# Performance work log

Hardware: AMD Instinct MI355X
Metric: run time of the kernel (lower is better)

## Reference

```python
import jax, jax.numpy as jnp
from jax import lax
import numpy as np

P = 16          # patch_len
EPS = 1e-5      # BatchNorm eps


def _dct_mats(L):
    # torch_dct DCT-II: ortho matrix Co and scale d s.t. dct(norm=None)(x) = (x @ Co.T) * d,
    # dct(norm='ortho')(x) = x @ Co.T, idct(norm=None)(y) = (y / d) @ Co
    n = jnp.arange(L, dtype=jnp.float32)
    base = jnp.cos(jnp.pi * (2.0 * n[None, :] + 1.0) * n[:, None] / (2.0 * L))
    ck = jnp.where(n == 0, 1.0 / jnp.sqrt(jnp.float32(L)), jnp.sqrt(2.0 / L))
    Co = base * ck[:, None]
    d = jnp.where(n == 0, 2.0 * jnp.sqrt(jnp.float32(L)), jnp.sqrt(2.0 * L))
    return Co, d


def _gelu(t):
    return jax.nn.gelu(t, approximate=False)  # torch nn.GELU default (erf)


def _dw(t, w, pad):  # depthwise Conv1d, t [B,D,L], w [D,k], SAME-style padding
    return lax.conv_general_dilated(t, w[:, None, :], (1,), [(pad, pad)],
                                    feature_group_count=t.shape[1],
                                    dimension_numbers=('NCH', 'OIH', 'NCH'))


def _forward(x, conv1_w, conv1_b, conv2_w, conv2_b, conv3_w, conv3_b,
             dn_g, dn_b, dn_m, dn_v, pn_g, pn_b, pn_m, pn_v,
             embed_w, embed_b, lin_res_w, lin_res_b,
             depth_res_w, depth_res_b, depth_conv_w, depth_conv_b,
             threshold, att_dw_w, att_dw_b, att_conv_w, att_conv_b,
             att_g, att_b, att_m, att_v, fc1_w, fc1_b, fc2_w, fc2_b):
    B, L, D = x.shape
    N = L // P                       # patch_num (stride == patch_len)
    Co, dvec = _dct_mats(L)

    conv1 = lambda t: t * conv1_w[:, None] + conv1_b[:, None]   # grouped 1x1 Conv1d
    bnD = lambda t: (t - dn_m[:, None]) * (dn_g[:, None] / jnp.sqrt(dn_v[:, None] + EPS)) + dn_b[:, None]

    xt = jnp.transpose(x, (0, 2, 1))                 # [B,D,L]
    freq_res = conv1(xt)
    z_dct = (xt @ Co.T) * dvec                       # dct(norm=None)

    # adaptive high-frequency mask
    energy = jnp.sum(z_dct * z_dct, axis=-1)         # [B,D]
    med = jnp.median(energy, axis=1, keepdims=True)
    ne = energy / (med + 1e-6)
    thr = lax.stop_gradient(jnp.quantile(ne, jnp.clip(threshold[0], 0.0, 1.0)))
    mask = (ne > thr).astype(x.dtype)[..., None]     # rows of dominant vars -> 1
    z = _gelu(conv1(z_dct * mask))
    z1 = (z / dvec) @ Co + freq_res                  # idct(norm=None) + residual

    # patching (stride == patch_len -> unfold is a reshape)
    z_p = xt.reshape(B * D, N, P) @ embed_w + embed_b            # [BD,N,P*P]
    z_res = (z_p.reshape(B, D, -1) @ lin_res_w + lin_res_b).transpose(0, 2, 1)  # [B,pred,D]
    time_res = z_p @ depth_res_w + depth_res_b                   # [BD,N,P]
    # depth_conv: grouped Conv1d kernel=stride=P over d_model=P*P
    z_depth = jnp.einsum('bnpj,nj->bnp', z_p.reshape(B * D, N, P, P), depth_conv_w) \
              + depth_conv_b[None, :, None] + time_res
    z_depth = (z_depth - pn_m[:, None]) * (pn_g[:, None] / jnp.sqrt(pn_v[:, None] + EPS)) + pn_b[:, None]
    z2 = _gelu(z_depth).reshape(B, D, L)

    z2_f = conv1(bnD(_gelu((z2 @ Co.T) * dvec)))

    z_r = jax.nn.sigmoid(conv1(bnD(_gelu(_dw(z1, conv2_w, 2) + conv2_b[:, None]))))
    zg = _gelu(z2_f * z_r)

    z1b = _gelu(bnD(_dw(z1, conv3_w, 3) + conv3_b[:, None]))
    z1c = bnD(zg) + z1b

    # DctAtt on z1c * z2: ortho DCT, take 5 low-freq comps per var
    xa = (z1c * z2) @ Co.T                            # [B,D,L]
    low = xa[:, :, :5].reshape(B, D, 5)               # concat layout matches torch loop
    zd = jnp.einsum('bdj,j->bd', low, att_dw_w) + att_dw_b[0]   # Conv1d(1,1,5,stride=5)
    zd = _gelu(zd)
    zd = (zd - att_m[0]) * (att_g[0] / jnp.sqrt(att_v[0] + EPS)) + att_b[0]  # BN(1)
    zd = zd * att_conv_w[0] + att_conv_b[0]           # Conv1d(1,1,1)
    att1 = jax.nn.softmax(zd, axis=-1)[..., None]     # [B,D,1]

    zf = z1c * att1 + z2 * (1.0 - att1)
    out = _gelu(zf @ fc1_w + fc1_b) @ fc2_w + fc2_b   # Mlp -> [B,D,pred]
    return z_res + out.transpose(0, 2, 1)             # [B,pred,D]


def setup_inputs() -> dict:
    key = jax.random.key(0)
    ks = iter(jax.random.split(key, 48))
    B, L, D, pred = 32, 512, 321, 96
    N, dm = L // P, P * P
    r = lambda shape, s=1.0: jax.random.normal(next(ks), shape, jnp.float32) * s
    return dict(
        x=r((B, L, D)),
        conv1_w=r((D,), 0.5) + 1.0, conv1_b=r((D,), 0.1),
        conv2_w=r((D, 5), 0.3), conv2_b=r((D,), 0.1),
        conv3_w=r((D, 7), 0.3), conv3_b=r((D,), 0.1),
        dn_g=jnp.ones((D,), jnp.float32), dn_b=jnp.zeros((D,), jnp.float32),
        dn_m=r((D,), 0.1), dn_v=jnp.ones((D,), jnp.float32),
        pn_g=jnp.ones((N,), jnp.float32), pn_b=jnp.zeros((N,), jnp.float32),
        pn_m=r((N,), 0.1), pn_v=jnp.ones((N,), jnp.float32),
        embed_w=r((P, dm), 0.25), embed_b=r((dm,), 0.02),
        lin_res_w=r((N * dm, pred), 0.01), lin_res_b=r((pred,), 0.02),
        depth_res_w=r((dm, P), 0.06), depth_res_b=r((P,), 0.02),
        depth_conv_w=r((N, P), 0.25), depth_conv_b=r((N,), 0.02),
        threshold=jax.random.uniform(next(ks), (1,), jnp.float32) * 0.5,
        att_dw_w=r((5,), 0.4), att_dw_b=r((1,), 0.1),
        att_conv_w=r((1,)), att_conv_b=r((1,), 0.1),
        att_g=jnp.ones((1,), jnp.float32), att_b=jnp.zeros((1,), jnp.float32),
        att_m=jnp.zeros((1,), jnp.float32), att_v=jnp.ones((1,), jnp.float32),
        fc1_w=r((L, pred), 0.04), fc1_b=r((pred,), 0.02),
        fc2_w=r((pred, pred), 0.1), fc2_b=r((pred,), 0.02),
    )


def reference(x, conv1_w, conv1_b, conv2_w, conv2_b, conv3_w, conv3_b,
              dn_g, dn_b, dn_m, dn_v, pn_g, pn_b, pn_m, pn_v,
              embed_w, embed_b, lin_res_w, lin_res_b,
              depth_res_w, depth_res_b, depth_conv_w, depth_conv_b,
              threshold, att_dw_w, att_dw_b, att_conv_w, att_conv_b,
              att_g, att_b, att_m, att_v, fc1_w, fc1_b, fc2_w, fc2_b):
    return _forward(x, conv1_w, conv1_b, conv2_w, conv2_b, conv3_w, conv3_b,
                    dn_g, dn_b, dn_m, dn_v, pn_g, pn_b, pn_m, pn_v,
                    embed_w, embed_b, lin_res_w, lin_res_b,
                    depth_res_w, depth_res_b, depth_conv_w, depth_conv_b,
                    threshold, att_dw_w, att_dw_b, att_conv_w, att_conv_b,
                    att_g, att_b, att_m, att_v, fc1_w, fc1_b, fc2_w, fc2_b)
```

## Files before the change

kernel.cpp:

```cpp
#include <hip/hip_runtime.h>
#include <cmath>


#define BB   32
#define LL   512
#define DD   321
#define PRED 96
#define M_ROWS (BB*DD)

__device__ __forceinline__ float gelu_f(float x){
  return 0.5f*x*(1.0f + erff(x*0.70710678118654752440f));
}
__device__ __forceinline__ float sigmoid_f(float x){
  return 1.0f/(1.0f+expf(-x));
}

constexpr size_t OFF_CO   = 0;
constexpr size_t OFF_COT  = OFF_CO   + 512*512;
constexpr size_t OFF_DVEC = OFF_COT  + 512*512;
constexpr size_t OFF_CATT = OFF_DVEC + 512;
constexpr size_t OFF_FC1T = OFF_CATT + 512;
constexpr size_t OFF_WEFFT= OFF_FC1T + 96*512;
constexpr size_t OFF_CRES = OFF_WEFFT+ 96*512;
constexpr size_t OFF_MP   = OFF_CRES + 128;
constexpr size_t OFF_C2P  = OFF_MP   + 32*256;
constexpr size_t OFF_AF   = OFF_C2P  + 512;
constexpr size_t OFF_CF   = OFF_AF   + 384;
constexpr size_t OFF_DNS  = OFF_CF   + 384;
constexpr size_t OFF_BF   = OFF_DNS  + 384;
constexpr size_t OFF_EN   = OFF_BF   + 384;
constexpr size_t OFF_NE   = OFF_EN   + 10368;
constexpr size_t OFF_THR  = OFF_NE   + 10368;
constexpr size_t OFF_ZDP  = OFF_THR  + 64;
constexpr size_t OFF_ATT1 = OFF_ZDP  + 10368;
constexpr size_t OFF_XT   = OFF_ATT1 + 10368;
constexpr size_t OFF_ZDCT = OFF_XT   + (size_t)M_ROWS*512;
constexpr size_t OFF_Z1   = OFF_ZDCT + (size_t)M_ROWS*512;
constexpr size_t OFF_Z2   = OFF_Z1   + (size_t)M_ROWS*512;
constexpr size_t OFF_Z1C  = OFF_Z2   + (size_t)M_ROWS*512;
constexpr size_t OFF_H    = OFF_Z1C  + (size_t)M_ROWS*512;
constexpr size_t OFF_ZRES = OFF_H    + (size_t)M_ROWS*96;
constexpr size_t WS_FLOATS= OFF_ZRES + (size_t)M_ROWS*96;

__global__ __launch_bounds__(256)
void k0_dct(float* __restrict__ Co, float* __restrict__ CoT, float* __restrict__ dvec,
            float* __restrict__ catt, const float* __restrict__ attw)
{
  const float PI_F = 3.14159265358979323846f;
  int b = blockIdx.x;
  float ckb = (b==0) ? (1.0f/sqrtf(512.0f)) : sqrtf(2.0f/512.0f);
  for (int l=threadIdx.x; l<512; l+=256){
    float a1 = PI_F * (float)(2*l+1);
    float a2 = a1 * (float)b;
    float c  = cosf(a2 * (1.0f/1024.0f)) * ckb;
    Co[b*512+l] = c;
  }
  for (int k=threadIdx.x; k<512; k+=256){
    float ckk = (k==0) ? (1.0f/sqrtf(512.0f)) : sqrtf(2.0f/512.0f);
    float a1 = PI_F * (float)(2*b+1);
    float a2 = a1 * (float)k;
    CoT[b*512+k] = cosf(a2 * (1.0f/1024.0f)) * ckk;
  }
  if (threadIdx.x==0) dvec[b] = (b==0) ? 2.0f*sqrtf(512.0f) : sqrtf(2.0f*512.0f);
  if (b==0){
    for (int l=threadIdx.x; l<512; l+=256){
      float sacc=0.f;
      for (int j=0;j<5;j++){
        float ckj = (j==0)?(1.0f/sqrtf(512.0f)):sqrtf(2.0f/512.0f);
        float a1 = PI_F*(float)(2*l+1);
        float a2 = a1*(float)j;
        sacc += cosf(a2 * (1.0f/1024.0f))*ckj*attw[j];
      }
      catt[l]=sacc;
    }
  }
}

__global__ __launch_bounds__(128)
void k0_weff(const float* __restrict__ embed_w, const float* __restrict__ embed_b,
             const float* __restrict__ lrw, const float* __restrict__ lrb,
             const float* __restrict__ fc1_w,
             float* __restrict__ fc1T, float* __restrict__ WeffT, float* __restrict__ cres)
{
  int l = blockIdx.x; int pr = threadIdx.x;
  if (l < 512){
    if (pr < 96){
      int n = l>>4, p = l&15;
      float a0=0.f,a1=0.f,a2=0.f,a3=0.f;
      for (int j=0;j<256;j+=4){
        a0 = fmaf(embed_w[p*256+j+0], lrw[((size_t)(n*256+j+0))*96+pr], a0);
        a1 = fmaf(embed_w[p*256+j+1], lrw[((size_t)(n*256+j+1))*96+pr], a1);
        a2 = fmaf(embed_w[p*256+j+2], lrw[((size_t)(n*256+j+2))*96+pr], a2);
        a3 = fmaf(embed_w[p*256+j+3], lrw[((size_t)(n*256+j+3))*96+pr], a3);
      }
      WeffT[pr*512 + l] = (a0+a1)+(a2+a3);
      fc1T [pr*512 + l] = fc1_w[l*96+pr];
    }
  } else {
    if (pr < 96){
      float a0=lrb[pr], a1=0.f, a2=0.f, a3=0.f;
      for (int i=0;i<8192;i+=4){
        a0 = fmaf(embed_b[(i+0) & 255], lrw[(size_t)(i+0)*96+pr], a0);
        a1 = fmaf(embed_b[(i+1) & 255], lrw[(size_t)(i+1)*96+pr], a1);
        a2 = fmaf(embed_b[(i+2) & 255], lrw[(size_t)(i+2)*96+pr], a2);
        a3 = fmaf(embed_b[(i+3) & 255], lrw[(size_t)(i+3)*96+pr], a3);
      }
      cres[pr]=(a0+a1)+(a2+a3);
    }
  }
}

__global__ __launch_bounds__(256)
void k0_depth(const float* __restrict__ embed_w, const float* __restrict__ embed_b,
              const float* __restrict__ drw, const float* __restrict__ drb,
              const float* __restrict__ dcw, const float* __restrict__ dcb,
              const float* __restrict__ png, const float* __restrict__ pnb,
              const float* __restrict__ pnm, const float* __restrict__ pnv,
              float* __restrict__ Mp, float* __restrict__ c2p)
{
  int n = blockIdx.x; int tid = threadIdx.x;
  int q = tid>>4, p = tid&15;
  float acc = 0.f;
  for (int j=0;j<16;j++)  acc = fmaf(embed_w[q*256 + p*16 + j], dcw[n*16+j], acc);
  float wtr = 0.f;
  for (int j=0;j<256;j++) wtr = fmaf(embed_w[q*256 + j], drw[j*16+p], wtr);
  float sn = png[n]/sqrtf(pnv[n]+1e-5f);
  Mp[n*256 + q*16 + p] = (acc + wtr) * sn;
  if (q==0){
    float c = dcb[n];
    for (int j=0;j<16;j++)  c = fmaf(embed_b[p*16+j], dcw[n*16+j], c);
    float ctr = drb[p];
    for (int j=0;j<256;j++) ctr = fmaf(embed_b[j], drw[j*16+p], ctr);
    c += ctr;
    c2p[n*16+p] = (c - pnm[n])*sn + pnb[n];
  }
}

__global__ void k0_fold(const float* __restrict__ w1, const float* __restrict__ b1,
                        const float* __restrict__ g,  const float* __restrict__ bbq,
                        const float* __restrict__ mq, const float* __restrict__ vq,
                        float* __restrict__ Af, float* __restrict__ Cf,
                        float* __restrict__ dns, float* __restrict__ Bf)
{
  int d = blockIdx.x*256 + threadIdx.x;
  if (d >= DD) return;
  float s  = g[d]/sqrtf(vq[d]+1e-5f);
  float bf = bbq[d] - mq[d]*s;
  dns[d]=s; Bf[d]=bf; Af[d]=s*w1[d]; Cf[d]=bf*w1[d]+b1[d];
}

__global__ __launch_bounds__(256)
void k1_transpose(const float* __restrict__ x, float* __restrict__ xt)
{
  int b = blockIdx.z; int l0 = blockIdx.y*32; int d0 = blockIdx.x*32;
  __shared__ float t[32][33];
  int tid=threadIdx.x; int j = tid&31, i0 = tid>>5;
  for (int ii=0; ii<32; ii+=8){
    int l = l0 + i0+ii; int d = d0 + j;
    t[i0+ii][j] = (d<DD) ? x[((size_t)b*512 + l)*DD + d] : 0.f;
  }
  __syncthreads();
  for (int ii=0; ii<32; ii+=8){
    int d = d0 + i0+ii; int l = l0 + j;
    if (d<DD) xt[((size_t)b*DD+d)*512 + l] = t[j][i0+ii];
  }
}

template<int OP>
__global__ __launch_bounds__(256)
void gemm_nt(const float* __restrict__ A, const float* __restrict__ B,
             float* __restrict__ C, int M, int Ncols, int ldc,
             const float* __restrict__ p0, const float* __restrict__ p1,
             const float* __restrict__ p2, const float* __restrict__ p3)
{
  __shared__ float As[32][132];
  __shared__ float Bs[32][68];
  const int tid = threadIdx.x;
  const int tx = tid & 15, ty = tid >> 4;
  const int rb = blockIdx.y * 128, cb = blockIdx.x * 64;

  float acc[8][4];
  #pragma unroll
  for (int i=0;i<8;i++)
    #pragma unroll
    for (int j=0;j<4;j++) acc[i][j]=0.f;

  for (int kb=0; kb<512; kb+=32){
    #pragma unroll
    for (int i=0;i<4;i++){
      int idx = tid + i*256;
      int row = idx >> 3, k4 = (idx & 7)*4;
      float4 v = make_float4(0.f,0.f,0.f,0.f);
      int r = rb + row;
      if (r < M) v = *reinterpret_cast<const float4*>(A + (size_t)r*512 + kb + k4);
      As[k4+0][row]=v.x; As[k4+1][row]=v.y; As[k4+2][row]=v.z; As[k4+3][row]=v.w;
    }
    #pragma unroll
    for (int i=0;i<2;i++){
      int idx = tid + i*256;
      int row = idx >> 3, k4 = (idx & 7)*4;
      float4 v = make_float4(0.f,0.f,0.f,0.f);
      int c = cb + row;
      if (c < Ncols) v = *reinterpret_cast<const float4*>(B + (size_t)c*512 + kb + k4);
      Bs[k4+0][row]=v.x; Bs[k4+1][row]=v.y; Bs[k4+2][row]=v.z; Bs[k4+3][row]=v.w;
    }
    __syncthreads();
    #pragma unroll
    for (int kk=0; kk<32; kk++){
      const float4 a0 = *reinterpret_cast<const float4*>(&As[kk][ty*8]);
      const float4 a1 = *reinterpret_cast<const float4*>(&As[kk][ty*8+4]);
      const float4 b0 = *reinterpret_cast<const float4*>(&Bs[kk][tx*4]);
      float av[8]={a0.x,a0.y,a0.z,a0.w,a1.x,a1.y,a1.z,a1.w};
      float bv[4]={b0.x,b0.y,b0.z,b0.w};
      #pragma unroll
      for (int i=0;i<8;i++)
        #pragma unroll
        for (int j=0;j<4;j++) acc[i][j]=fmaf(av[i],bv[j],acc[i][j]);
    }
    __syncthreads();
  }

  #pragma unroll
  for (int i=0;i<8;i++){
    const int r = rb + ty*8 + i;
    const bool rok = (r < M);
    if constexpr (OP==0){
      if (rok){
        #pragma unroll
        for (int j=0;j<4;j++){
          int c = cb + tx*4 + j;
          C[(size_t)r*ldc + c] = acc[i][j]*p0[c];
        }
      }
    } else if constexpr (OP==1){
      if (rok){
        int d = r % DD;
        float w = p0[d], bo = p1[d];
        #pragma unroll
        for (int j=0;j<4;j++){
          int c = cb + tx*4 + j;
          C[(size_t)r*ldc + c] = acc[i][j] + p2[(size_t)r*512 + c]*w + bo;
        }
      }
    } else if constexpr (OP==2){
      if (rok){
        int d = r % DD;
        float w = p0[d], bo = p1[d];
        #pragma unroll
        for (int j=0;j<4;j++){
          int c = cb + tx*4 + j;
          float t = acc[i][j]*p3[c];
          C[(size_t)r*ldc + c] = gelu_f(t)*w + bo;
        }
      }
    } else if constexpr (OP==3){
      if (rok){
        #pragma unroll
        for (int j=0;j<4;j++){
          int c = cb + tx*4 + j;
          if (c < Ncols) C[(size_t)r*ldc + c] = gelu_f(acc[i][j] + p0[c]);
        }
      }
    } else {
      if (rok){
        #pragma unroll
        for (int j=0;j<4;j++){
          int c = cb + tx*4 + j;
          if (c < Ncols) C[(size_t)r*ldc + c] = acc[i][j] + p0[c];
        }
      }
    }
  }
}

__global__ __launch_bounds__(256)
void k_energy(const float* __restrict__ zdct, float* __restrict__ energy)
{
  int r=blockIdx.x, tid=threadIdx.x;
  __shared__ float rbuf[256];
  float acc=0.f;
  for (int k=tid;k<512;k+=256){ float v=zdct[(size_t)r*512+k]; acc=fmaf(v,v,acc); }
  rbuf[tid]=acc; __syncthreads();
  for (int st=128;st>0;st>>=1){ if(tid<st) rbuf[tid]+=rbuf[tid+st]; __syncthreads(); }
  if (tid==0) energy[r]=rbuf[0];
}

__global__ __launch_bounds__(256)
void k3_median(const float* __restrict__ energy, float* __restrict__ ne)
{
  int b = blockIdx.x, tid=threadIdx.x;
  __shared__ float e[DD];
  __shared__ float medv;
  for (int i=tid;i<DD;i+=256) e[i]=energy[b*DD+i];
  __syncthreads();
  for (int i=tid;i<DD;i+=256){
    float v=e[i]; int lt=0, eq=0;
    for (int j=0;j<DD;j++){ float u=e[j]; lt += (u<v); eq += (u==v); }
    if (lt<=160 && 160<lt+eq) medv=v;
  }
  __syncthreads();
  float den = medv + 1e-6f;
  for (int i=tid;i<DD;i+=256) ne[b*DD+i] = e[i]/den;
}

__global__ __launch_bounds__(1024)
void k3_thr(const float* __restrict__ ne, const float* __restrict__ thrin,
            float* __restrict__ out)
{
  __shared__ int hist[256];
  __shared__ unsigned sPrefix; __shared__ int sRank;
  int tid = threadIdx.x;
  float q = fminf(fmaxf(thrin[0],0.f),1.f);
  float pos = q * (float)(M_ROWS-1);
  int lo = (int)floorf(pos); int hi = (int)ceilf(pos);
  float frac = pos - floorf(pos);
  float vals[2];
  for (int s=0;s<2;s++){
    int rank = s ? hi : lo;
    unsigned prefix=0, pmask=0;
    for (int pass=0; pass<4; pass++){
      int shift = 24 - 8*pass;
      if (tid<256) hist[tid]=0;
      __syncthreads();
      for (int i=tid;i<M_ROWS;i+=1024){
        unsigned u = __float_as_uint(ne[i]);
        if ((u & pmask)==prefix) atomicAdd(&hist[(u>>shift)&255u],1);
      }
      __syncthreads();
      if (tid==0){
        int cum=0;
        for (int bkt=0;bkt<256;bkt++){
          int c=hist[bkt];
          if (cum + c > rank){ sPrefix = prefix | ((unsigned)bkt<<(unsigned)shift); sRank = rank - cum; break; }
          cum += c;
        }
      }
      __syncthreads();
      prefix = sPrefix; rank = sRank; pmask |= (0xFFu<<(unsigned)shift);
      __syncthreads();
    }
    vals[s] = __uint_as_float(prefix);
  }
  if (tid==0) out[0] = vals[0]*(1.0f-frac) + vals[1]*frac;
}

__global__ void k4_pre(float* __restrict__ zdct, const float* __restrict__ ne,
                       const float* __restrict__ thr, const float* __restrict__ w1,
                       const float* __restrict__ b1, const float* __restrict__ dvec)
{
  size_t idx = (size_t)blockIdx.x*256 + threadIdx.x;
  int r = (int)(idx>>7);
  int k0 = ((int)idx & 127)*4;
  float m  = (ne[r] > thr[0]) ? 1.f : 0.f;
  int d = r % DD;
  float w = w1[d]*m, bo = b1[d];
  float4 v = ((float4*)zdct)[idx];
  v.x = gelu_f(fmaf(v.x,w,bo))/dvec[k0+0];
  v.y = gelu_f(fmaf(v.y,w,bo))/dvec[k0+1];
  v.z = gelu_f(fmaf(v.z,w,bo))/dvec[k0+2];
  v.w = gelu_f(fmaf(v.w,w,bo))/dvec[k0+3];
  ((float4*)zdct)[idx]=v;
}

__global__ __launch_bounds__(256)
void k5_z2(const float* __restrict__ xt, const float* __restrict__ Mp,
           const float* __restrict__ c2p, float* __restrict__ z2)
{
  int r = blockIdx.x, tid=threadIdx.x;
  __shared__ float row[512];
  for (int i=tid;i<512;i+=256) row[i]=xt[(size_t)r*512+i];
  __syncthreads();
  for (int idx=tid; idx<512; idx+=256){
    int n = idx>>4, p = idx&15;
    float acc = c2p[idx];
    const float* Mn = Mp + n*256 + p;
    #pragma unroll
    for (int qq=0;qq<16;qq++) acc = fmaf(row[n*16+qq], Mn[qq*16], acc);
    z2[(size_t)r*512+idx] = gelu_f(acc);
  }
}

__global__ __launch_bounds__(256)
void k7_fuse(const float* __restrict__ z1, const float* __restrict__ z2f,
             const float* __restrict__ z2, float* __restrict__ z1c,
             float* __restrict__ zdpre,
             const float* __restrict__ c2w, const float* __restrict__ c2b,
             const float* __restrict__ c3w, const float* __restrict__ c3b,
             const float* __restrict__ Af,  const float* __restrict__ Cf,
             const float* __restrict__ dns, const float* __restrict__ Bf,
             const float* __restrict__ catt)
{
  int r = blockIdx.x, tid=threadIdx.x;
  int d = r % DD;
  __shared__ float zrow[518];
  __shared__ float rbuf[256];
  for (int i=tid;i<518;i+=256){
    int l = i-3;
    zrow[i] = (l>=0 && l<512) ? z1[(size_t)r*512+l] : 0.f;
  }
  __syncthreads();
  float w2[5], w3[7];
  #pragma unroll
  for (int t=0;t<5;t++) w2[t]=c2w[d*5+t];
  #pragma unroll
  for (int t=0;t<7;t++) w3[t]=c3w[d*7+t];
  const float cb2=c2b[d], cb3=c3b[d];
  const float af=Af[d], cf=Cf[d], s=dns[d], bf=Bf[d];
  float dotacc=0.f;
  for (int l=tid;l<512;l+=256){
    float c5=cb2;
    #pragma unroll
    for (int t=0;t<5;t++) c5 = fmaf(zrow[l+t+1], w2[t], c5);
    float zr  = sigmoid_f(fmaf(gelu_f(c5),af,cf));
    float zgv = gelu_f(z2f[(size_t)r*512+l]*zr);
    float c7=cb3;
    #pragma unroll
    for (int t=0;t<7;t++) c7 = fmaf(zrow[l+t], w3[t], c7);
    float z1b = gelu_f(fmaf(c7,s,bf));
    float v = fmaf(zgv,s,bf) + z1b;
    z1c[(size_t)r*512+l]=v;
    dotacc = fmaf(v*z2[(size_t)r*512+l], catt[l], dotacc);
  }
  rbuf[tid]=dotacc; __syncthreads();
  for (int st=128;st>0;st>>=1){ if(tid<st) rbuf[tid]+=rbuf[tid+st]; __syncthreads(); }
  if (tid==0) zdpre[r]=rbuf[0];
}

__global__ __launch_bounds__(256)
void k8_att(const float* __restrict__ zdpre, float* __restrict__ att1,
            const float* __restrict__ adwb, const float* __restrict__ acw,
            const float* __restrict__ acb,  const float* __restrict__ ag,
            const float* __restrict__ ab,   const float* __restrict__ am,
            const float* __restrict__ av)
{
  int b=blockIdx.x, t=threadIdx.x;
  __shared__ float sred[256];
  float vloc[2];
  float mx=-INFINITY;
  float sA = ag[0]/sqrtf(av[0]+1e-5f);
  #pragma unroll
  for (int ii=0;ii<2;ii++){
    int d=t+ii*256;
    float v=-INFINITY;
    if (d<DD){
      float zd = zdpre[b*DD+d] + adwb[0];
      zd = gelu_f(zd);
      zd = (zd-am[0])*sA + ab[0];
      zd = zd*acw[0] + acb[0];
      v=zd;
    }
    vloc[ii]=v; mx=fmaxf(mx,v);
  }
  sred[t]=mx; __syncthreads();
  for (int st=128;st>0;st>>=1){ if (t<st) sred[t]=fmaxf(sred[t],sred[t+st]); __syncthreads(); }
  float m=sred[0]; __syncthreads();
  float e0 = (t<DD)     ? expf(vloc[0]-m) : 0.f;
  float e1 = (t+256<DD) ? expf(vloc[1]-m) : 0.f;
  sred[t]=e0+e1; __syncthreads();
  for (int st=128;st>0;st>>=1){ if (t<st) sred[t]+=sred[t+st]; __syncthreads(); }
  float sum=sred[0];
  if (t<DD)     att1[b*DD+t]     = e0/sum;
  if (t+256<DD) att1[b*DD+t+256] = e1/sum;
}

__global__ void k8b_zf(const float* __restrict__ z1c, const float* __restrict__ z2,
                       const float* __restrict__ att1, float* __restrict__ zf)
{
  size_t idx = (size_t)blockIdx.x*256 + threadIdx.x;
  int r = (int)(idx>>7);
  float a = att1[r];
  float4 v1 = ((const float4*)z1c)[idx];
  float4 v2 = ((const float4*)z2)[idx];
  float4 o;
  o.x = v1.x*a + v2.x*(1.f-a);
  o.y = v1.y*a + v2.y*(1.f-a);
  o.z = v1.z*a + v2.z*(1.f-a);
  o.w = v1.w*a + v2.w*(1.f-a);
  ((float4*)zf)[idx]=o;
}

__global__ __launch_bounds__(256)
void k9_final(const float* __restrict__ h, const float* __restrict__ zres,
              const float* __restrict__ fc2_w, const float* __restrict__ fc2_b,
              float* __restrict__ outF)
{
  int b = blockIdx.y; int d0 = blockIdx.x*32;
  __shared__ float f2[96*96];
  __shared__ float hs[32][97];
  __shared__ float zs[32][97];
  int tid=threadIdx.x;
  for (int i=tid;i<96*96;i+=256) f2[i]=fc2_w[i];
  for (int i=tid;i<32*96;i+=256){
    int dl = i/96, p = i%96; int d = d0+dl;
    float hv=0.f, zv=0.f;
    if (d<DD){ hv = h[((size_t)b*DD+d)*96+p]; zv = zres[((size_t)b*DD+d)*96+p]; }
    hs[dl][p]=hv; zs[dl][p]=zv;
  }
  __syncthreads();
  int tx = tid & 31, ty = tid >> 5;
  int d = d0+tx;
  float acc[12];
  #pragma unroll
  for (int kc=0;kc<12;kc++) acc[kc]=0.f;
  for (int p=0;p<96;p++){
    float hv = hs[tx][p];
    #pragma unroll
    for (int kc=0;kc<12;kc++) acc[kc] = fmaf(hv, f2[p*96 + ty + kc*8], acc[kc]);
  }
  if (d<DD){
    #pragma unroll
    for (int kc=0;kc<12;kc++){
      int c = ty + kc*8;
      outF[((size_t)b*96 + c)*DD + d] = acc[kc] + fc2_b[c] + zs[tx][c];
    }
  }
}

extern "C" void kernel_launch(void* const* d_in, const int* in_sizes, int n_in,
                              void* d_out, int out_size, void* d_ws, size_t ws_size,
                              hipStream_t stream)
{
  (void)in_sizes; (void)n_in; (void)out_size; (void)ws_size;
  const float* x        =(const float*)d_in[0];
  const float* conv1_w  =(const float*)d_in[1];
  const float* conv1_b  =(const float*)d_in[2];
  const float* conv2_w  =(const float*)d_in[3];
  const float* conv2_b  =(const float*)d_in[4];
  const float* conv3_w  =(const float*)d_in[5];
  const float* conv3_b  =(const float*)d_in[6];
  const float* dn_g     =(const float*)d_in[7];
  const float* dn_b     =(const float*)d_in[8];
  const float* dn_m     =(const float*)d_in[9];
  const float* dn_v     =(const float*)d_in[10];
  const float* pn_g     =(const float*)d_in[11];
  const float* pn_b     =(const float*)d_in[12];
  const float* pn_m     =(const float*)d_in[13];
  const float* pn_v     =(const float*)d_in[14];
  const float* embed_w  =(const float*)d_in[15];
  const float* embed_b  =(const float*)d_in[16];
  const float* lin_res_w=(const float*)d_in[17];
  const float* lin_res_b=(const float*)d_in[18];
  const float* depth_res_w=(const float*)d_in[19];
  const float* depth_res_b=(const float*)d_in[20];
  const float* depth_conv_w=(const float*)d_in[21];
  const float* depth_conv_b=(const float*)d_in[22];
  const float* threshold=(const float*)d_in[23];
  const float* att_dw_w =(const float*)d_in[24];
  const float* att_dw_b =(const float*)d_in[25];
  const float* att_conv_w=(const float*)d_in[26];
  const float* att_conv_b=(const float*)d_in[27];
  const float* att_g    =(const float*)d_in[28];
  const float* att_b    =(const float*)d_in[29];
  const float* att_m    =(const float*)d_in[30];
  const float* att_v    =(const float*)d_in[31];
  const float* fc1_w    =(const float*)d_in[32];
  const float* fc1_b    =(const float*)d_in[33];
  const float* fc2_w    =(const float*)d_in[34];
  const float* fc2_b    =(const float*)d_in[35];

  float* ws   = (float*)d_ws;
  float* Co   = ws + OFF_CO;
  float* CoT  = ws + OFF_COT;
  float* dvec = ws + OFF_DVEC;
  float* catt = ws + OFF_CATT;
  float* fc1T = ws + OFF_FC1T;
  float* WeffT= ws + OFF_WEFFT;
  float* cres = ws + OFF_CRES;
  float* Mp   = ws + OFF_MP;
  float* c2p  = ws + OFF_C2P;
  float* Af   = ws + OFF_AF;
  float* Cf   = ws + OFF_CF;
  float* dns  = ws + OFF_DNS;
  float* Bf   = ws + OFF_BF;
  float* energy=ws + OFF_EN;
  float* ne   = ws + OFF_NE;
  float* thr  = ws + OFF_THR;
  float* zdpre= ws + OFF_ZDP;
  float* att1 = ws + OFF_ATT1;
  float* xt   = ws + OFF_XT;
  float* zdct = ws + OFF_ZDCT;
  float* z1   = ws + OFF_Z1;
  float* z2   = ws + OFF_Z2;
  float* z1c  = ws + OFF_Z1C;
  float* h    = ws + OFF_H;
  float* zres = ws + OFF_ZRES;

  k0_dct  <<<512, 256, 0, stream>>>(Co, CoT, dvec, catt, att_dw_w);
  k0_weff <<<513, 128, 0, stream>>>(embed_w, embed_b, lin_res_w, lin_res_b, fc1_w,
                                    fc1T, WeffT, cres);
  k0_depth<<<32, 256, 0, stream>>>(embed_w, embed_b, depth_res_w, depth_res_b,
                                   depth_conv_w, depth_conv_b, pn_g, pn_b, pn_m, pn_v,
                                   Mp, c2p);
  k0_fold <<<2, 256, 0, stream>>>(conv1_w, conv1_b, dn_g, dn_b, dn_m, dn_v,
                                  Af, Cf, dns, Bf);

  k1_transpose<<<dim3(11,16,BB), 256, 0, stream>>>(x, xt);
  gemm_nt<0><<<dim3(8,81), 256, 0, stream>>>(xt, Co, zdct, M_ROWS, 512, 512,
                                             dvec, nullptr, nullptr, nullptr);
  k_energy <<<M_ROWS, 256, 0, stream>>>(zdct, energy);
  k3_median<<<BB, 256, 0, stream>>>(energy, ne);
  k3_thr   <<<1, 1024, 0, stream>>>(ne, threshold, thr);

  k4_pre   <<<5136, 256, 0, stream>>>(zdct, ne, thr, conv1_w, conv1_b, dvec);
  gemm_nt<1><<<dim3(8,81), 256, 0, stream>>>(zdct, CoT, z1, M_ROWS, 512, 512,
                                             conv1_w, conv1_b, xt, nullptr);

  k5_z2    <<<M_ROWS, 256, 0, stream>>>(xt, Mp, c2p, z2);
  gemm_nt<2><<<dim3(8,81), 256, 0, stream>>>(z2, Co, zdct, M_ROWS, 512, 512,
                                             Af, Cf, nullptr, dvec);

  k7_fuse  <<<M_ROWS, 256, 0, stream>>>(z1, zdct, z2, z1c, zdpre,
                                        conv2_w, conv2_b, conv3_w, conv3_b,
                                        Af, Cf, dns, Bf, catt);
  k8_att   <<<BB, 256, 0, stream>>>(zdpre, att1, att_dw_b, att_conv_w, att_conv_b,
                                    att_g, att_b, att_m, att_v);
  k8b_zf   <<<5136, 256, 0, stream>>>(z1c, z2, att1, z1);

  gemm_nt<3><<<dim3(2,81), 256, 0, stream>>>(z1, fc1T, h, M_ROWS, 96, 96,
                                             fc1_b, nullptr, nullptr, nullptr);
  gemm_nt<4><<<dim3(2,81), 256, 0, stream>>>(xt, WeffT, zres, M_ROWS, 96, 96,
                                             cres, nullptr, nullptr, nullptr);
  k9_final <<<dim3(11,BB), 256, 0, stream>>>(h, zres, fc2_w, fc2_b, (float*)d_out);
}
```

Before: 898.1 us.

## Restructure effective-weight precompute into tiled split-K kernel with reduction pass

Replaces the per-row weight-folding kernel, which re-read lin_res_w from global memory for each output and ran one serial 8192-long bias dot product in a single block, with a shared-memory tiled kernel split over patches and four K chunks. Partial results and bias partials are reduced by a small finalize kernel. The fc1 transpose moves to its own coalesced shared-memory transpose kernel. This adds two launches and some workspace for partials in exchange for far less redundant global traffic and a shorter serial tail.

```diff
diff --git a/kernel.cpp b/kernel.cpp
--- a/kernel.cpp
+++ b/kernel.cpp
@@ -40,7 +40,9 @@
 constexpr size_t OFF_Z1C  = OFF_Z2   + (size_t)M_ROWS*512;
 constexpr size_t OFF_H    = OFF_Z1C  + (size_t)M_ROWS*512;
 constexpr size_t OFF_ZRES = OFF_H    + (size_t)M_ROWS*96;
-constexpr size_t WS_FLOATS= OFF_ZRES + (size_t)M_ROWS*96;
+constexpr size_t OFF_WPART= OFF_ZRES + (size_t)M_ROWS*96;
+constexpr size_t OFF_PCRES= OFF_WPART+ 4*96*512;
+constexpr size_t WS_FLOATS= OFF_PCRES+ 128*96;
 
 __global__ __launch_bounds__(256)
 void k0_dct(float* __restrict__ Co, float* __restrict__ CoT, float* __restrict__ dvec,
@@ -76,37 +78,83 @@
   }
 }
 
-__global__ __launch_bounds__(128)
-void k0_weff(const float* __restrict__ embed_w, const float* __restrict__ embed_b,
-             const float* __restrict__ lrw, const float* __restrict__ lrb,
-             const float* __restrict__ fc1_w,
-             float* __restrict__ fc1T, float* __restrict__ WeffT, float* __restrict__ cres)
-{
-  int l = blockIdx.x; int pr = threadIdx.x;
-  if (l < 512){
+__global__ __launch_bounds__(256)
+void kA_weff(const float* __restrict__ ew_g, const float* __restrict__ eb_g,
+             const float* __restrict__ lrw,
+             float* __restrict__ Wpart, float* __restrict__ pcres)
+{
+  const int n = blockIdx.x, kb4 = blockIdx.y;
+  __shared__ float ews[16][68];
+  __shared__ float ebs[64];
+  __shared__ float lw[64][96];
+  const int tid = threadIdx.x;
+  const int jbase = kb4*64;
+  for (int i=tid; i<1024; i+=256){
+    int p2 = i>>6, j2 = i&63;
+    ews[p2][j2] = ew_g[p2*256 + jbase + j2];
+  }
+  if (tid < 64) ebs[tid] = eb_g[jbase + tid];
+  for (int i=tid; i<1536; i+=256){
+    int jj = i/24, c4 = i%24;
+    *(float4*)&lw[jj][c4*4] =
+      *(const float4*)&lrw[((size_t)(n*256 + jbase + jj))*96 + c4*4];
+  }
+  __syncthreads();
+  const int p = tid>>4, tx = tid&15;
+  float acc[6]={0,0,0,0,0,0};
+  float accB[6]={0,0,0,0,0,0};
+  for (int jj=0; jj<64; jj++){
+    float a = ews[p][jj];
+    #pragma unroll
+    for (int g=0; g<6; g++) acc[g] = fmaf(a, lw[jj][tx+16*g], acc[g]);
+    if (p==0){
+      float bv = ebs[jj];
+      #pragma unroll
+      for (int g=0; g<6; g++) accB[g] = fmaf(bv, lw[jj][tx+16*g], accB[g]);
+    }
+  }
+  #pragma unroll
+  for (int g=0; g<6; g++){
+    int pr = tx + 16*g;
+    Wpart[((size_t)kb4*96 + pr)*512 + n*16 + p] = acc[g];
+    if (p==0) pcres[(n*4+kb4)*96 + pr] = accB[g];
+  }
+}
+
+__global__ __launch_bounds__(256)
+void kA_fin(const float* __restrict__ Wpart, const float* __restrict__ pcres,
+            const float* __restrict__ lrb,
+            float* __restrict__ WeffT, float* __restrict__ cres)
+{
+  int b = blockIdx.x;
+  if (b < 192){
+    int i = b*256 + threadIdx.x;
+    WeffT[i] = (Wpart[i] + Wpart[49152+i]) + (Wpart[2*49152+i] + Wpart[3*49152+i]);
+  } else {
+    int pr = threadIdx.x;
     if (pr < 96){
-      int n = l>>4, p = l&15;
-      float a0=0.f,a1=0.f,a2=0.f,a3=0.f;
-      for (int j=0;j<256;j+=4){
-        a0 = fmaf(embed_w[p*256+j+0], lrw[((size_t)(n*256+j+0))*96+pr], a0);
-        a1 = fmaf(embed_w[p*256+j+1], lrw[((size_t)(n*256+j+1))*96+pr], a1);
-        a2 = fmaf(embed_w[p*256+j+2], lrw[((size_t)(n*256+j+2))*96+pr], a2);
-        a3 = fmaf(embed_w[p*256+j+3], lrw[((size_t)(n*256+j+3))*96+pr], a3);
-      }
-      WeffT[pr*512 + l] = (a0+a1)+(a2+a3);
-      fc1T [pr*512 + l] = fc1_w[l*96+pr];
-    }
-  } else {
-    if (pr < 96){
-      float a0=lrb[pr], a1=0.f, a2=0.f, a3=0.f;
-      for (int i=0;i<8192;i+=4){
-        a0 = fmaf(embed_b[(i+0) & 255], lrw[(size_t)(i+0)*96+pr], a0);
-        a1 = fmaf(embed_b[(i+1) & 255], lrw[(size_t)(i+1)*96+pr], a1);
-        a2 = fmaf(embed_b[(i+2) & 255], lrw[(size_t)(i+2)*96+pr], a2);
-        a3 = fmaf(embed_b[(i+3) & 255], lrw[(size_t)(i+3)*96+pr], a3);
-      }
-      cres[pr]=(a0+a1)+(a2+a3);
-    }
+      float s = lrb[pr];
+      for (int nn=0; nn<128; nn++) s += pcres[nn*96+pr];
+      cres[pr] = s;
+    }
+  }
+}
+
+__global__ __launch_bounds__(256)
+void kT_fc1(const float* __restrict__ fc1_w, float* __restrict__ fc1T)
+{
+  __shared__ float t[32][33];
+  int c0 = blockIdx.x*32;
+  int l0 = blockIdx.y*32;
+  int tid=threadIdx.x; int j=tid&31, i0=tid>>5;
+  for (int ii=0; ii<32; ii+=8){
+    int l=l0+i0+ii, c=c0+j;
+    t[i0+ii][j] = (c<96)? fc1_w[l*96+c] : 0.f;
+  }
+  __syncthreads();
+  for (int ii=0; ii<32; ii+=8){
+    int c=c0+i0+ii, l=l0+j;
+    if (c<96) fc1T[(size_t)c*512 + l] = t[j][i0+ii];
   }
 }
 
@@ -584,10 +632,13 @@
   float* z1c  = ws + OFF_Z1C;
   float* h    = ws + OFF_H;
   float* zres = ws + OFF_ZRES;
+  float* Wpart= ws + OFF_WPART;
+  float* pcres= ws + OFF_PCRES;
 
   k0_dct  <<<512, 256, 0, stream>>>(Co, CoT, dvec, catt, att_dw_w);
-  k0_weff <<<513, 128, 0, stream>>>(embed_w, embed_b, lin_res_w, lin_res_b, fc1_w,
-                                    fc1T, WeffT, cres);
+  kA_weff <<<dim3(32,4), 256, 0, stream>>>(embed_w, embed_b, lin_res_w, Wpart, pcres);
+  kA_fin  <<<193, 256, 0, stream>>>(Wpart, pcres, lin_res_b, WeffT, cres);
+  kT_fc1  <<<dim3(3,16), 256, 0, stream>>>(fc1_w, fc1T);
   k0_depth<<<32, 256, 0, stream>>>(embed_w, embed_b, depth_res_w, depth_res_b,
                                    depth_conv_w, depth_conv_b, pn_g, pn_b, pn_m, pn_v,
                                    Mp, c2p);
```

Measured after the change: 792.8 us. 11.7% less time.
